# Kernel tuning notes

Measured on AMD Instinct MI355X. Metric: run time of the kernel, lower is better.

## Reference

```python
import jax, jax.numpy as jnp
import numpy as np

M1, M2 = 16, 16  # Fourier modes per dim


def conv1x1(x, w, b):
    # x: [B,Ci,H,W], w: [Co,Ci], b: [Co]
    return jnp.einsum('bihw,oi->bohw', x, w) + b[None, :, None, None]


def fno_block(x, wr, wi, bw, bb):
    # x: [B,C,H,W]; wr/wi: [C,C,M1,M2]; bw: [C,C]; bb: [C]
    H, W = x.shape[-2], x.shape[-1]
    x_fft = jnp.fft.rfftn(x, axes=(-2, -1), norm='ortho')[:, :, :M1, :M2]
    w = (wr + 1j * wi).astype(jnp.complex64)
    out_fft = jnp.einsum('bikl,iokl->bokl', x_fft, w)
    # irfftn with s zero-pads truncated modes back to full spatial size
    x_spec = jnp.fft.irfftn(out_fft, s=(H, W), axes=(-2, -1), norm='ortho')
    return jax.nn.gelu(x_spec + conv1x1(x, bw, bb), approximate=False)


def setup_inputs() -> dict:
    key = jax.random.key(0)
    ks = jax.random.split(key, 8)
    B, in_c, H, W = 4, 3, 256, 256
    out_c, n_blocks, width = 4, 4, 32
    scale = 1.0 / (width * width)
    return {
        'x': jax.random.normal(ks[0], (B, in_c, H, W), jnp.float32),
        'lift_w': jax.random.normal(ks[1], (width, in_c), jnp.float32) * 0.1,
        'lift_b': jnp.zeros((width,), jnp.float32),
        'wr': jax.random.normal(ks[2], (out_c, n_blocks, width, width, M1, M2), jnp.float32) * scale,
        'wi': jax.random.normal(ks[3], (out_c, n_blocks, width, width, M1, M2), jnp.float32) * scale,
        'byp_w': jax.random.normal(ks[4], (out_c, n_blocks, width, width), jnp.float32) * 0.1,
        'byp_b': jnp.zeros((out_c, n_blocks, width), jnp.float32),
        'proj_w': jax.random.normal(ks[5], (1, width), jnp.float32) * 0.1,
        'proj_b': jnp.zeros((1,), jnp.float32),
    }


def reference(x, lift_w, lift_b, wr, wi, byp_w, byp_b, proj_w, proj_b):
    out_c, n_blocks = wr.shape[0], wr.shape[1]
    x0 = conv1x1(x, lift_w, lift_b)
    outputs = []
    for o in range(out_c):
        xb = x0
        for n in range(n_blocks):
            xb = fno_block(xb, wr[o, n], wi[o, n], byp_w[o, n], byp_b[o, n])
        outputs.append(conv1x1(xb, proj_w, proj_b))
    return jnp.concatenate(outputs, axis=1)
```

## Files before the change

### kernel.cpp

```cpp
#include <hip/hip_runtime.h>
#include <hip/hip_bf16.h>

#define NB 4
#define NC 32
#define NH 256
#define NW 256
#define NM 16
constexpr int NPIX = NH * NW;
constexpr int NP = NB * NC * NPIX;
constexpr int ZG = NB * NC * NM * NM * 2;

typedef short bf16x8 __attribute__((ext_vector_type(8)));
typedef float f32x4  __attribute__((ext_vector_type(4)));
typedef unsigned short u16;
typedef unsigned int u32;

#define MFMA16(a, b, c) __builtin_amdgcn_mfma_f32_16x16x32_bf16(a, b, c, 0, 0, 0)

__device__ __forceinline__ u16 f2bf(float f) {
    const __hip_bfloat16 h = __float2bfloat16(f);
    return __builtin_bit_cast(u16, h);
}
__device__ __forceinline__ float bf2f(u16 h) {
    return __uint_as_float(((unsigned)h) << 16);
}
__device__ __forceinline__ u32 packsplit(float f) {
    const u16 hi = f2bf(f);
    const u16 lo = f2bf(f - bf2f(hi));
    return (u32)hi | ((u32)lo << 16);
}

__device__ __forceinline__ float gelu_fast(float v) {
    const float ax = fabsf(v) * 0.70710678118654752f;
    const float t = __builtin_amdgcn_rcpf(1.0f + 0.3275911f * ax);
    const float y = t * (0.254829592f + t * (-0.284496736f + t * (1.421413741f +
                    t * (-1.453152027f + t * 1.061405429f))));
    const float e = __expf(-ax * ax);
    float er = 1.0f - y * e;
    er = copysignf(er, v);
    return 0.5f * v * (1.0f + er);
}

__global__ __launch_bounds__(256) void tab_prep(
    u16* __restrict__ cwhi, u16* __restrict__ cwlo,
    u16* __restrict__ ebhi, u16* __restrict__ eblo)
{
    const int id = blockIdx.x * 256 + threadIdx.x;
    if (id < 8192) {
        const int nn = id >> 5, k = id & 31;
        const int m = ((k & 15) * nn) & 255;
        float s, c;
        sincospif((float)m * (2.0f / 256.0f), &s, &c);
        const float v = (k < 16) ? c : s;
        const u16 hi = f2bf(v);
        cwhi[id] = hi;
        cwlo[id] = f2bf(v - bf2f(hi));
    } else {
        const int id2 = id - 8192;
        const int row = id2 >> 8, w = id2 & 255;
        const int m = ((row & 15) * w) & 255;
        float s, c;
        sincospif((float)m * (2.0f / 256.0f), &s, &c);
        const float v = 0.0625f * ((row < 16) ? c : s);
        const u16 hi = f2bf(v);
        ebhi[id2] = hi;
        eblo[id2] = f2bf(v - bf2f(hi));
    }
}

__global__ __launch_bounds__(256) void s1_lift(
    const float* __restrict__ src,
    const float* __restrict__ lift_w,
    const float* __restrict__ lift_b,
    const u16* __restrict__ ebhi,
    const u16* __restrict__ eblo,
    u32* __restrict__ ypk)
{
    __shared__ u32 TrPk[64][33];

    const int tid = threadIdx.x;
    const int c  = blockIdx.x;
    const int b  = blockIdx.y;
    const int hq = blockIdx.z;
    const int wv = tid >> 6, lane = tid & 63;
    const int mrow = lane & 15, q = lane >> 4;
    const int hbase = hq * 64 + wv * 16;

    const float lw0 = lift_w[c * 3 + 0], lw1 = lift_w[c * 3 + 1], lw2 = lift_w[c * 3 + 2];
    const float lb = lift_b[c];
    const float* sb = src + (size_t)b * 3 * NPIX;

    f32x4 acc[2] = {};
    for (int ks = 0; ks < 8; ++ks) {
        bf16x8 bh[2], bl[2];
        #pragma unroll
        for (int nt = 0; nt < 2; ++nt) {
            const int off = (nt * 16 + mrow) * 256 + ks * 32 + q * 8;
            bh[nt] = *(const bf16x8*)(ebhi + off);
            bl[nt] = *(const bf16x8*)(eblo + off);
        }
        const float* xp = sb + (size_t)(hbase + mrow) * NW + ks * 32 + q * 8;
        const float4 p0a = *(const float4*)(xp);
        const float4 p0b = *(const float4*)(xp + 4);
        const float4 p1a = *(const float4*)(xp + NPIX);
        const float4 p1b = *(const float4*)(xp + NPIX + 4);
        const float4 p2a = *(const float4*)(xp + 2 * NPIX);
        const float4 p2b = *(const float4*)(xp + 2 * NPIX + 4);
        float v[8];
        v[0] = lw0 * p0a.x + lw1 * p1a.x + lw2 * p2a.x + lb;
        v[1] = lw0 * p0a.y + lw1 * p1a.y + lw2 * p2a.y + lb;
        v[2] = lw0 * p0a.z + lw1 * p1a.z + lw2 * p2a.z + lb;
        v[3] = lw0 * p0a.w + lw1 * p1a.w + lw2 * p2a.w + lb;
        v[4] = lw0 * p0b.x + lw1 * p1b.x + lw2 * p2b.x + lb;
        v[5] = lw0 * p0b.y + lw1 * p1b.y + lw2 * p2b.y + lb;
        v[6] = lw0 * p0b.z + lw1 * p1b.z + lw2 * p2b.z + lb;
        v[7] = lw0 * p0b.w + lw1 * p1b.w + lw2 * p2b.w + lb;
        bf16x8 xh, xl;
        #pragma unroll
        for (int j = 0; j < 8; ++j) {
            const u16 hi = f2bf(v[j]);
            xh[j] = (short)hi;
            xl[j] = (short)f2bf(v[j] - bf2f(hi));
        }
        #pragma unroll
        for (int nt = 0; nt < 2; ++nt) {
            acc[nt] = MFMA16(xh, bh[nt], acc[nt]);
            acc[nt] = MFMA16(xh, bl[nt], acc[nt]);
            acc[nt] = MFMA16(xl, bh[nt], acc[nt]);
        }
    }

    #pragma unroll
    for (int nt = 0; nt < 2; ++nt) {
        #pragma unroll
        for (int r = 0; r < 4; ++r)
            TrPk[wv * 16 + q * 4 + r][nt * 16 + mrow] = packsplit(acc[nt][r]);
    }
    __syncthreads();

    #pragma unroll
    for (int i = 0; i < 8; ++i) {
        const int idx = i * 256 + tid;
        const int hl = idx >> 5, combo = idx & 31;
        ypk[((size_t)b * 256 + hq * 64 + hl) * 1024 + c * 32 + combo] = TrPk[hl][combo];
    }
}

__global__ __launch_bounds__(256) void s2_kernel(
    const u32* __restrict__ ypk,
    const u16* __restrict__ ebhi,
    const u16* __restrict__ eblo,
    float* __restrict__ zred)
{
    __shared__ u32 Yl[256][33];
    __shared__ float P[32][33];

    const int tid = threadIdx.x;
    const int c  = blockIdx.x;
    const int gb = blockIdx.y;
    const int wv = tid >> 6, lane = tid & 63;
    const int mrow = lane & 15, q = lane >> 4;

    #pragma unroll
    for (int i = 0; i < 32; ++i) {
        const int idx = i * 256 + tid;
        const int h = idx >> 5, combo = idx & 31;
        Yl[h][combo] = ypk[((size_t)gb * 256 + h) * 1024 + c * 32 + combo];
    }
    __syncthreads();

    const int mt2 = wv >> 1, nt2 = wv & 1;
    const int wc = nt2 * 16 + mrow;
    f32x4 p = {};
    for (int ks = 0; ks < 8; ++ks) {
        const int aoff = (mt2 * 16 + mrow) * 256 + ks * 32 + q * 8;
        const bf16x8 ah = *(const bf16x8*)(ebhi + aoff);
        const bf16x8 al = *(const bf16x8*)(eblo + aoff);
        bf16x8 yh, yl;
        #pragma unroll
        for (int j = 0; j < 8; ++j) {
            const u32 v = Yl[ks * 32 + q * 8 + j][wc];
            yh[j] = (short)(v & 0xFFFFu);
            yl[j] = (short)(v >> 16);
        }
        p = MFMA16(ah, yh, p);
        p = MFMA16(ah, yl, p);
        p = MFMA16(al, yh, p);
    }
    #pragma unroll
    for (int r = 0; r < 4; ++r)
        P[mt2 * 16 + q * 4 + r][wc] = p[r];
    __syncthreads();

    const int k = tid >> 4, l = tid & 15;
    const float zr = P[k][l] - P[16 + k][16 + l];
    const float zi = -(P[k][16 + l] + P[16 + k][l]);
    const int idx = (gb * NC + c) * 256 + tid;
    zred[idx * 2 + 0] = zr;
    zred[idx * 2 + 1] = zi;
}

__global__ __launch_bounds__(256) void mix_kernel(
    const float* __restrict__ zred,
    float* __restrict__ zmix,
    const float* __restrict__ wr,
    const float* __restrict__ wi,
    int o0, int n, int zgmul)
{
    __shared__ float ps[4][NB][64][2];
    const int tid = threadIdx.x;
    const int oc = blockIdx.x, mq = blockIdx.y, g = blockIdx.z;
    const int o = o0 + g, zg = zgmul * g;
    const int ichunk = tid >> 6, ml = tid & 63;
    const int mode = mq * 64 + ml;

    const float* wrb = wr + (size_t)(o * 4 + n) * NC * NC * 256;
    const float* wib = wi + (size_t)(o * 4 + n) * NC * NC * 256;

    float orr[NB] = {0.f, 0.f, 0.f, 0.f};
    float oii[NB] = {0.f, 0.f, 0.f, 0.f};

    #pragma unroll
    for (int ii = 0; ii < 8; ++ii) {
        const int i = ichunk * 8 + ii;
        const float wrv = wrb[(i * NC + oc) * 256 + mode];
        const float wiv = wib[(i * NC + oc) * 256 + mode];
        #pragma unroll
        for (int b = 0; b < NB; ++b) {
            const float2 z = *(const float2*)&zred[(((zg * NB + b) * NC + i) * 256 + mode) * 2];
            orr[b] += z.x * wrv - z.y * wiv;
            oii[b] += z.x * wiv + z.y * wrv;
        }
    }
    #pragma unroll
    for (int b = 0; b < NB; ++b) {
        ps[ichunk][b][ml][0] = orr[b];
        ps[ichunk][b][ml][1] = oii[b];
    }
    __syncthreads();

    const int b2 = tid >> 6, ml2 = tid & 63;
    float re = 0.f, im = 0.f;
    #pragma unroll
    for (int ic = 0; ic < 4; ++ic) {
        re += ps[ic][b2][ml2][0];
        im += ps[ic][b2][ml2][1];
    }
    const int oidx = ((g * NB + b2) * NC + oc) * 256 + mq * 64 + ml2;
    zmix[oidx * 2 + 0] = re;
    zmix[oidx * 2 + 1] = im;
}

template<bool LIFT, bool FINAL, bool PRODY>
__global__ __launch_bounds__(256) void inv_kernel(
    const float* __restrict__ zmix,
    const void* srcv,
    const float* __restrict__ byp_w,
    const float* __restrict__ byp_b,
    const float* __restrict__ lift_w,
    const float* __restrict__ lift_b,
    const float* __restrict__ proj_w,
    const float* __restrict__ proj_b,
    const u16* __restrict__ cwhi,
    const u16* __restrict__ cwlo,
    const u16* __restrict__ ebhi,
    const u16* __restrict__ eblo,
    u32* __restrict__ ypk,
    void* dstv,
    int o0, int n)
{
    __shared__ float2 tw[256];
    __shared__ u16 Thi[NC * 40], Tlo[NC * 40];
    __shared__ u16 Whi[NC * 40], Wlo[NC * 40];
    __shared__ float bbl[NC];
    __shared__ float bweffs[NC * 3];
    __shared__ u16 Ghi[PRODY ? 32 * 264 : 1];
    __shared__ u16 Glo[PRODY ? 32 * 264 : 1];
    __shared__ u32 Ypks[PRODY ? 1024 : 1];

    const int tid = threadIdx.x;
    const int h = blockIdx.x;
    const int gb = blockIdx.y;
    const int g = gb >> 2, b = gb & 3;
    const int o = o0 + g;

    {
        float s, cs;
        sincospif((float)tid * (2.0f / 256.0f), &s, &cs);
        tw[tid] = make_float2(cs, s);
    }

    const float* bwp = byp_w + (size_t)(o * 4 + n) * NC * NC;
    const float* bbp = byp_b + (o * 4 + n) * NC;

    if (LIFT) {
        if (tid < 96) {
            const int oc = tid / 3, j = tid % 3;
            float s = 0.f;
            for (int ic = 0; ic < NC; ++ic) s += bwp[oc * NC + ic] * lift_w[ic * 3 + j];
            bweffs[oc * 3 + j] = s;
        } else if (tid < 128) {
            const int oc = tid - 96;
            float s = bbp[oc];
            for (int ic = 0; ic < NC; ++ic) s += bwp[oc * NC + ic] * lift_b[ic];
            bbl[oc] = s;
        }
    } else {
        if (tid < NC) bbl[tid] = bbp[tid];
    }
    __syncthreads();

    for (int idx = tid; idx < NC * NC; idx += 256) {
        const int c = idx >> 5, ic = idx & 31;
        float v;
        if (LIFT) v = (ic < 3) ? bweffs[c * 3 + ic] : 0.f;
        else      v = bwp[idx];
        const u16 hi = f2bf(v);
        Whi[c * 40 + ic] = hi;
        Wlo[c * 40 + ic] = f2bf(v - bf2f(hi));
    }

    #pragma unroll
    for (int rep = 0; rep < 2; ++rep) {
        const int it = rep * 256 + tid;
        const int c = it >> 4, l = it & 15;
        const float sl = (l == 0 ? 1.0f : 2.0f) / 256.0f;
        const float* zp = zmix + ((size_t)(gb * NC + c) * 256 + l) * 2;
        float tr = 0.f, ti = 0.f;
        int m = 0;
        #pragma unroll
        for (int k = 0; k < NM; ++k) {
            const float2 z = *(const float2*)(zp + k * 32);
            const float2 t = tw[m];
            tr += z.x * t.x - z.y * t.y;
            ti += z.x * t.y + z.y * t.x;
            m = (m + h) & 255;
        }
        tr *= sl; ti *= sl;
        if (l == 0) tr += bbl[c];
        const u16 rh = f2bf(tr);
        Thi[c * 40 + l] = rh;
        Tlo[c * 40 + l] = f2bf(tr - bf2f(rh));
        const float nti_ = -ti;
        const u16 ih = f2bf(nti_);
        Thi[c * 40 + 16 + l] = ih;
        Tlo[c * 40 + 16 + l] = f2bf(nti_ - bf2f(ih));
    }
    __syncthreads();

    const int lane = tid & 63, wv = tid >> 6;
    const int mrow = lane & 15, q = lane >> 4;

    bf16x8 aThi[2], aTlo[2], aWhi[2], aWlo[2];
    #pragma unroll
    for (int mt = 0; mt < 2; ++mt) {
        const int ro = (mt * 16 + mrow) * 40 + 8 * q;
        aThi[mt] = *(const bf16x8*)&Thi[ro];
        aTlo[mt] = *(const bf16x8*)&Tlo[ro];
        aWhi[mt] = *(const bf16x8*)&Whi[ro];
        aWlo[mt] = *(const bf16x8*)&Wlo[ro];
    }

    float pwv[8];
    float pb = 0.f;
    if (FINAL) {
        #pragma unroll
        for (int mt = 0; mt < 2; ++mt)
            #pragma unroll
            for (int i = 0; i < 4; ++i)
                pwv[mt * 4 + i] = proj_w[mt * 16 + q * 4 + i];
        pb = proj_b[0];
    }

    const float* xbf = LIFT ? (const float*)srcv + (size_t)b * 3 * NPIX + h * NW : nullptr;
    const u32*   xbp = LIFT ? nullptr : (const u32*)srcv + (size_t)gb * NC * NPIX + h * NW;
    u32*   dstp = (u32*)dstv;
    float* dstf = (float*)dstv;

    u32 cur[8];
    if (!LIFT) {
        const int ncol0 = (wv * 4 + 0) * 16 + mrow;
        #pragma unroll
        for (int j = 0; j < 8; ++j)
            cur[j] = xbp[(size_t)(8 * q + j) * NPIX + ncol0];
    }

    #pragma unroll
    for (int nti = 0; nti < 4; ++nti) {
        const int nt = wv * 4 + nti;
        const int ncol = nt * 16 + mrow;

        const bf16x8 cwh = *(const bf16x8*)(cwhi + ncol * 32 + 8 * q);
        const bf16x8 cwl = *(const bf16x8*)(cwlo + ncol * 32 + 8 * q);

        u32 nxt[8];
        if (!LIFT && nti < 3) {
            const int ncoln = (nt + 1) * 16 + mrow;
            #pragma unroll
            for (int j = 0; j < 8; ++j)
                nxt[j] = xbp[(size_t)(8 * q + j) * NPIX + ncoln];
        }

        bf16x8 xh, xl;
        #pragma unroll
        for (int j = 0; j < 8; ++j) {
            if (LIFT) {
                const int k = 8 * q + j;
                const float v = (k < 3) ? xbf[(size_t)k * NPIX + ncol] : 0.f;
                const u16 hi = f2bf(v);
                xh[j] = (short)hi;
                xl[j] = (short)f2bf(v - bf2f(hi));
            } else {
                xh[j] = (short)(cur[j] & 0xFFFFu);
                xl[j] = (short)(cur[j] >> 16);
            }
        }

        float fpart = 0.f;
        #pragma unroll
        for (int mt = 0; mt < 2; ++mt) {
            f32x4 accT = {0.f, 0.f, 0.f, 0.f};
            f32x4 accW = {0.f, 0.f, 0.f, 0.f};
            accT = MFMA16(aThi[mt], cwh, accT);
            accT = MFMA16(aThi[mt], cwl, accT);
            accT = MFMA16(aTlo[mt], cwh, accT);
            accW = MFMA16(aWhi[mt], xh, accW);
            accW = MFMA16(aWhi[mt], xl, accW);
            accW = MFMA16(aWlo[mt], xh, accW);
            const f32x4 acc = accT + accW;
            if (FINAL) {
                #pragma unroll
                for (int i = 0; i < 4; ++i)
                    fpart += gelu_fast(acc[i]) * pwv[mt * 4 + i];
            } else {
                #pragma unroll
                for (int i = 0; i < 4; ++i) {
                    const int c = mt * 16 + q * 4 + i;
                    const float gl = gelu_fast(acc[i]);
                    dstp[((size_t)gb * NC + c) * NPIX + h * NW + ncol] = packsplit(gl);
                    if (PRODY) {
                        const u16 hi = f2bf(gl);
                        Ghi[c * 264 + ncol] = hi;
                        Glo[c * 264 + ncol] = f2bf(gl - bf2f(hi));
                    }
                }
            }
        }
        if (FINAL) {
            fpart += __shfl_xor(fpart, 16);
            fpart += __shfl_xor(fpart, 32);
            if (q == 0) {
                dstf[(((size_t)b * 4 + o) * NH + h) * NW + nt * 16 + mrow] = fpart + pb;
            }
        }

        if (!LIFT && nti < 3) {
            #pragma unroll
            for (int j = 0; j < 8; ++j) cur[j] = nxt[j];
        }
    }

    if (PRODY) {
        __syncthreads();
        const int mt1 = wv >> 1, nt1 = wv & 1;
        f32x4 yA = {}, yB = {}, yC = {};
        #pragma unroll
        for (int ks = 0; ks < 8; ++ks) {
            const int ao = (mt1 * 16 + mrow) * 264 + ks * 32 + q * 8;
            const bf16x8 gh = *(const bf16x8*)&Ghi[ao];
            const bf16x8 gl = *(const bf16x8*)&Glo[ao];
            const int bo = (nt1 * 16 + mrow) * 256 + ks * 32 + q * 8;
            const bf16x8 bh = *(const bf16x8*)(ebhi + bo);
            const bf16x8 bl = *(const bf16x8*)(eblo + bo);
            yA = MFMA16(gh, bh, yA);
            yB = MFMA16(gh, bl, yB);
            yC = MFMA16(gl, bh, yC);
        }
        const f32x4 yacc = yA + yB + yC;
        #pragma unroll
        for (int r = 0; r < 4; ++r) {
            const int c = mt1 * 16 + q * 4 + r;
            const int combo = nt1 * 16 + mrow;
            Ypks[c * 32 + combo] = packsplit(yacc[r]);
        }
        __syncthreads();
        u32* yout = ypk + ((size_t)gb * 256 + h) * 1024;
        #pragma unroll
        for (int i = 0; i < 4; ++i)
            yout[i * 256 + tid] = Ypks[i * 256 + tid];
    }
}

extern "C" void kernel_launch(void* const* d_in, const int* in_sizes, int n_in,
                              void* d_out, int out_size, void* d_ws, size_t ws_size,
                              hipStream_t stream)
{
    const float* x      = (const float*)d_in[0];
    const float* lift_w = (const float*)d_in[1];
    const float* lift_b = (const float*)d_in[2];
    const float* wr     = (const float*)d_in[3];
    const float* wi     = (const float*)d_in[4];
    const float* byp_w  = (const float*)d_in[5];
    const float* byp_b  = (const float*)d_in[6];
    const float* proj_w = (const float*)d_in[7];
    const float* proj_b = (const float*)d_in[8];
    float* ws  = (float*)d_ws;

    auto need_bytes = [](int Gq) -> size_t {
        size_t bts = 0;
        bts += (size_t)4 * 8192 * sizeof(u16);
        bts += (size_t)65536 * 4;
        bts += (size_t)4 * 256 * 1024 * 4;
        bts += (size_t)Gq * NB * 256 * 1024 * 4;
        bts += (size_t)Gq * ZG * 4 * 2;
        bts += (size_t)Gq * NP * 4;
        return bts;
    };
    const int G = (ws_size >= need_bytes(4)) ? 4 : 2;

    u16* cwhi = (u16*)ws;
    u16* cwlo = cwhi + 8192;
    u16* ebhi = cwlo + 8192;
    u16* eblo = ebhi + 8192;
    float* zlift = ws + 16384;
    u32* ylift = (u32*)(zlift + 65536);
    u32* y     = ylift + (size_t)4 * 256 * 1024;
    float* zred = (float*)(y + (size_t)G * NB * 256 * 1024);
    float* zmix = zred + (size_t)G * ZG;
    u32* buf  = (u32*)(zmix + (size_t)G * ZG);

    tab_prep<<<64, 256, 0, stream>>>(cwhi, cwlo, ebhi, eblo);

    s1_lift<<<dim3(NC, NB, 4), 256, 0, stream>>>(x, lift_w, lift_b, ebhi, eblo, ylift);
    s2_kernel<<<dim3(NC, NB), 256, 0, stream>>>(ylift, ebhi, eblo, zlift);

    for (int o0 = 0; o0 < 4; o0 += G) {
        for (int n = 0; n < 4; ++n) {
            const bool lift = (n == 0);
            const bool fin  = (n == 3);

            if (!lift)
                s2_kernel<<<dim3(NC, G * NB), 256, 0, stream>>>(y, ebhi, eblo, zred);

            mix_kernel<<<dim3(NC, 4, G), 256, 0, stream>>>(
                lift ? zlift : zred, zmix, wr, wi, o0, n, lift ? 0 : 1);

            dim3 igrid(NH, G * NB);
            if (fin) {
                inv_kernel<false, true, false><<<igrid, 256, 0, stream>>>(
                    zmix, buf, byp_w, byp_b, lift_w, lift_b, proj_w, proj_b,
                    cwhi, cwlo, ebhi, eblo, y, d_out, o0, n);
            } else if (lift) {
                inv_kernel<true, false, true><<<igrid, 256, 0, stream>>>(
                    zmix, x, byp_w, byp_b, lift_w, lift_b, proj_w, proj_b,
                    cwhi, cwlo, ebhi, eblo, y, buf, o0, n);
            } else {
                inv_kernel<false, false, true><<<igrid, 256, 0, stream>>>(
                    zmix, buf, byp_w, byp_b, lift_w, lift_b, proj_w, proj_b,
                    cwhi, cwlo, ebhi, eblo, y, buf, o0, n);
            }
        }
    }
}
```

Measured before the change: 446.2 us.

## Store intermediate activations channel-last to enable vectorized loads and stores

Switches the packed hi/lo activation buffer from channel-major [B,C,H,W] to pixel-major [B,H,W,C]. Each lane can then fetch its 8 channels with two 16-byte loads and write its 4 output channels with one 16-byte store, replacing scattered 4-byte accesses strided by NPIX. This cuts memory transactions in the pointwise/GELU stage. Any other kernel that reads this buffer (forward FFT or projection stages) must use the same layout, and the change to packsplit-derived LDS values assumes packsplit packs hi in the low half.

```diff
diff --git a/kernel.cpp b/kernel.cpp
--- a/kernel.cpp
+++ b/kernel.cpp
@@ -373,16 +373,16 @@
     }
 
     const float* xbf = LIFT ? (const float*)srcv + (size_t)b * 3 * NPIX + h * NW : nullptr;
-    const u32*   xbp = LIFT ? nullptr : (const u32*)srcv + (size_t)gb * NC * NPIX + h * NW;
+    const u32*   xbp = LIFT ? nullptr : (const u32*)srcv + ((size_t)gb * NH + h) * NW * NC;
     u32*   dstp = (u32*)dstv;
+    u32*   drow = FINAL ? nullptr : dstp + ((size_t)gb * NH + h) * NW * NC;
     float* dstf = (float*)dstv;
 
-    u32 cur[8];
+    uint4 curA, curB;
     if (!LIFT) {
-        const int ncol0 = (wv * 4 + 0) * 16 + mrow;
-        #pragma unroll
-        for (int j = 0; j < 8; ++j)
-            cur[j] = xbp[(size_t)(8 * q + j) * NPIX + ncol0];
+        const int ncol0 = wv * 64 + mrow;
+        curA = *(const uint4*)(xbp + ncol0 * NC + 8 * q);
+        curB = *(const uint4*)(xbp + ncol0 * NC + 8 * q + 4);
     }
 
     #pragma unroll
@@ -393,26 +393,30 @@
         const bf16x8 cwh = *(const bf16x8*)(cwhi + ncol * 32 + 8 * q);
         const bf16x8 cwl = *(const bf16x8*)(cwlo + ncol * 32 + 8 * q);
 
-        u32 nxt[8];
+        uint4 nxtA, nxtB;
         if (!LIFT && nti < 3) {
             const int ncoln = (nt + 1) * 16 + mrow;
+            nxtA = *(const uint4*)(xbp + ncoln * NC + 8 * q);
+            nxtB = *(const uint4*)(xbp + ncoln * NC + 8 * q + 4);
+        }
+
+        bf16x8 xh, xl;
+        if (LIFT) {
             #pragma unroll
-            for (int j = 0; j < 8; ++j)
-                nxt[j] = xbp[(size_t)(8 * q + j) * NPIX + ncoln];
-        }
-
-        bf16x8 xh, xl;
-        #pragma unroll
-        for (int j = 0; j < 8; ++j) {
-            if (LIFT) {
+            for (int j = 0; j < 8; ++j) {
                 const int k = 8 * q + j;
                 const float v = (k < 3) ? xbf[(size_t)k * NPIX + ncol] : 0.f;
                 const u16 hi = f2bf(v);
                 xh[j] = (short)hi;
                 xl[j] = (short)f2bf(v - bf2f(hi));
-            } else {
-                xh[j] = (short)(cur[j] & 0xFFFFu);
-                xl[j] = (short)(cur[j] >> 16);
+            }
+        } else {
+            const u32 cw8[8] = {curA.x, curA.y, curA.z, curA.w,
+                                curB.x, curB.y, curB.z, curB.w};
+            #pragma unroll
+            for (int j = 0; j < 8; ++j) {
+                xh[j] = (short)(cw8[j] & 0xFFFFu);
+                xl[j] = (short)(cw8[j] >> 16);
             }
         }
 
@@ -433,17 +437,20 @@
                 for (int i = 0; i < 4; ++i)
                     fpart += gelu_fast(acc[i]) * pwv[mt * 4 + i];
             } else {
+                uint4 st;
+                u32* stw = (u32*)&st;
                 #pragma unroll
                 for (int i = 0; i < 4; ++i) {
                     const int c = mt * 16 + q * 4 + i;
                     const float gl = gelu_fast(acc[i]);
-                    dstp[((size_t)gb * NC + c) * NPIX + h * NW + ncol] = packsplit(gl);
+                    const u32 pk = packsplit(gl);
+                    stw[i] = pk;
                     if (PRODY) {
-                        const u16 hi = f2bf(gl);
-                        Ghi[c * 264 + ncol] = hi;
-                        Glo[c * 264 + ncol] = f2bf(gl - bf2f(hi));
+                        Ghi[c * 264 + ncol] = (u16)(pk & 0xFFFFu);
+                        Glo[c * 264 + ncol] = (u16)(pk >> 16);
                     }
                 }
+                *(uint4*)(drow + ncol * NC + mt * 16 + q * 4) = st;
             }
         }
         if (FINAL) {
@@ -455,8 +462,8 @@
         }
 
         if (!LIFT && nti < 3) {
-            #pragma unroll
-            for (int j = 0; j < 8; ++j) cur[j] = nxt[j];
+            curA = nxtA;
+            curB = nxtB;
         }
     }
 
```

Result: slower. 462.2 us (+3.6%).
